# Kernel optimization log

Measured on AMD Instinct MI355X. Metric: run time of the kernel, lower is better.

Reference implementation:

```python
import jax, jax.numpy as jnp
import numpy as np

# Dimensions
B, T = 128, 512
H = 256            # lstm_hiddens; encoder width is 2*H
LIN = 200          # linear_hiddens (LSTMCell input size)
PD, WD = 50, 20    # pos_dims, wordlen_dims
PN, WN = 32, 8     # pos_num, wordlen_num (word len clipped to 7)
SP = 58            # segpos_num
APP_ID = 0         # id of the APP action (forbidden at t=0)


def setup_inputs() -> dict:
    key = jax.random.key(0)
    ks = jax.random.split(key, 13)
    enc = jax.random.normal(ks[0], (B, T, 2 * H), dtype=jnp.float32)
    sep_mask = jax.random.randint(ks[1], (B, T), 0, 2, dtype=jnp.int32)
    sep_mask = sep_mask.at[:, 0].set(1)  # first action is always SEP (APP forbidden at t=0)
    pos_ids = jax.random.randint(ks[2], (B, T), 0, PN, dtype=jnp.int32)
    length = jax.random.randint(ks[3], (B,), T // 2, T + 1, dtype=jnp.int32)
    s = 0.05
    pos_emb = jax.random.normal(ks[4], (PN, PD), dtype=jnp.float32) * s
    wordlen_emb = jax.random.normal(ks[5], (WN, WD), dtype=jnp.float32) * s
    fc_W = jax.random.normal(ks[6], (LIN, PD + 2 * H + WD), dtype=jnp.float32) * s
    fc_b = jax.random.normal(ks[7], (LIN,), dtype=jnp.float32) * s
    W_ih = jax.random.normal(ks[8], (4 * H, LIN), dtype=jnp.float32) * s
    W_hh = jax.random.normal(ks[9], (4 * H, H), dtype=jnp.float32) * s
    b_ih = jax.random.normal(ks[10], (4 * H,), dtype=jnp.float32) * s
    b_hh = jax.random.normal(ks[11], (4 * H,), dtype=jnp.float32) * s
    combine_W = jax.random.normal(ks[12], (SP, 3 * H), dtype=jnp.float32) * s
    return {"encoder_output": enc, "sep_mask": sep_mask, "pos_ids": pos_ids,
            "length": length, "pos_emb": pos_emb, "wordlen_emb": wordlen_emb,
            "fc_W": fc_W, "fc_b": fc_b, "W_ih": W_ih, "W_hh": W_hh,
            "b_ih": b_ih, "b_hh": b_hh, "combine_W": combine_W}


def reference(encoder_output, sep_mask, pos_ids, length, pos_emb, wordlen_emb,
              fc_W, fc_b, W_ih, W_hh, b_ih, b_hh, combine_W):
    b, t, h2 = encoder_output.shape
    h = h2 // 2
    idx = jnp.arange(t, dtype=jnp.int32)

    # last SEP position strictly before t (word start of the in-progress word)
    sep_pos = jnp.where(sep_mask > 0, idx[None, :], 0)            # [B,T]
    cmax = jax.lax.cummax(sep_pos, axis=1)                        # last sep <= t
    last_sep = jnp.concatenate(
        [jnp.zeros((b, 1), jnp.int32), cmax[:, :-1]], axis=1)     # last sep < t

    wlen = idx[None, :] - last_sep                                # [B,T]; >=1 for t>=1
    wlen_safe = jnp.maximum(wlen, 1)
    wlen_id = jnp.minimum(wlen_safe, 7)                           # clip: len>6 -> 7

    # mean of encoder states over the current word [last_sep, t) via cumsum
    csum = jnp.concatenate(
        [jnp.zeros((b, 1, h2), encoder_output.dtype),
         jnp.cumsum(encoder_output, axis=1)], axis=1)             # [B,T+1,2H]
    start_sum = jnp.take_along_axis(csum, last_sep[:, :, None], axis=1)
    word_avg = (csum[:, :t] - start_sum) / wlen_safe[:, :, None].astype(encoder_output.dtype)

    last_pos = jnp.take_along_axis(pos_ids, last_sep, axis=1)     # [B,T]
    feats = jnp.concatenate(
        [pos_emb[last_pos], word_avg, wordlen_emb[wlen_id]], axis=-1)  # [B,T,PD+2H+WD]
    z = jnp.tanh(jnp.einsum('btf,lf->btl', feats, fc_W) + fc_b)   # [B,T,LIN]
    z = z.at[:, 0].set(0.0)                                       # step 0 input is zeros

    # LSTMCell recurrence over time (torch gate order: i, f, g, o)
    def step(carry, zt):
        hh, cc = carry
        g = zt @ W_ih.T + b_ih + hh @ W_hh.T + b_hh               # [B,4H]
        i, f, gg, o = jnp.split(g, 4, axis=-1)
        cc = jax.nn.sigmoid(f) * cc + jax.nn.sigmoid(i) * jnp.tanh(gg)
        hh = jax.nn.sigmoid(o) * jnp.tanh(cc)
        return (hh, cc), hh

    h0 = jnp.zeros((b, h), encoder_output.dtype)
    _, hs = jax.lax.scan(step, (h0, h0), jnp.swapaxes(z, 0, 1))   # hs: [T,B,H]
    hs = jnp.swapaxes(hs, 0, 1)                                   # [B,T,H]

    v = jnp.concatenate([hs, encoder_output], axis=-1)            # [B,T,3H]
    logits = jnp.einsum('btv,sv->bts', v, combine_W)              # [B,T,SP]
    logits = logits.at[:, 0, APP_ID].set(-1e30)                   # forbid APP at t=0 (in-place, no grad)
    valid = (idx[None, :] < length[:, None])[:, :, None]
    logits = jnp.where(valid, logits, 0.0)                        # pad steps emit zeros
    return logits.reshape(b * t, SP)
```

## Files before the change

### kernel.cpp

```cpp
#include <hip/hip_runtime.h>

typedef unsigned short ushort_t;
typedef unsigned int uint32;
typedef __attribute__((ext_vector_type(8))) short short8;
typedef __attribute__((ext_vector_type(4))) short short4v;
typedef __attribute__((ext_vector_type(4))) float floatx4;
typedef __attribute__((ext_vector_type(2))) float float2v;
typedef __attribute__((ext_vector_type(8))) int intx8;

#define B_    128
#define T_    512
#define H_    256
#define H2_   512
#define LIN_  200
#define LINP_ 224
#define G4_   1024
#define SP_   58
#define BT_   (B_*T_)

#define OFF_LS     0UL
#define OFF_LP     262144UL
#define OFF_WID    524288UL
#define OFF_INV    786432UL
#define OFF_POSW   1212416UL
#define OFF_WLW    1238016UL
#define OFF_BIASG  1244416UL
#define OFF_WHH    1248512UL
#define OFF_WIH    1772800UL
#define OFF_WENC   2231552UL
#define OFF_COMBW  2436352UL
#define OFF_ECW    2525440UL
#define OFF_Z      28739840UL
#define OFF_GPERM  58099968UL
#define OFF_VBF    192317696UL

__device__ __forceinline__ ushort_t f2bf(float x){
  uint32 u = __float_as_uint(x);
  u += 0x7fffu + ((u >> 16) & 1u);
  return (ushort_t)(u >> 16);
}
__device__ __forceinline__ float bf2f(ushort_t v){
  return __uint_as_float(((uint32)v) << 16);
}
__device__ __forceinline__ float fsig(float x){
  return __builtin_amdgcn_rcpf(1.0f + __expf(-x));
}
__device__ __forceinline__ float ftanh(float x){
  return 1.0f - 2.0f * __builtin_amdgcn_rcpf(1.0f + __expf(2.0f * x));
}

__global__ __launch_bounds__(512) void k_scan(const int* __restrict__ sep, const int* __restrict__ pos_ids,
                       int* __restrict__ ls, int* __restrict__ lp,
                       int* __restrict__ wid, float* __restrict__ inv){
  int b = blockIdx.x, t = threadIdx.x;
  __shared__ int sm[512];
  int v = (sep[b*T_ + t] > 0) ? t : 0;
  sm[t] = v;
  __syncthreads();
  #pragma unroll
  for (int off = 1; off < 512; off <<= 1){
    int o = (t >= off) ? sm[t - off] : 0;
    __syncthreads();
    v = (o > v) ? o : v;
    sm[t] = v;
    __syncthreads();
  }
  int l = (t == 0) ? 0 : sm[t - 1];
  int wlen = t - l;
  int wsv  = (wlen < 1) ? 1 : wlen;
  ls[b*T_ + t]  = l;
  lp[b*T_ + t]  = pos_ids[b*T_ + l];
  wid[b*T_ + t] = (wsv > 7) ? 7 : wsv;
  inv[b*T_ + t] = 1.0f / (float)wsv;
}

__global__ __launch_bounds__(256) void k_encbf(const float* __restrict__ enc, ushort_t* __restrict__ vbf){
  const long total = (long)BT_ * 128;
  for (long i = (long)blockIdx.x * 256 + threadIdx.x; i < total; i += 2048L * 256){
    floatx4 v = ((const floatx4*)enc)[i];
    long row = i >> 7;
    int c4 = (int)(i & 127);
    int b = (int)(row >> 9), t = (int)(row & (T_-1));
    short4v pk;
    pk[0] = (short)f2bf(v[0]); pk[1] = (short)f2bf(v[1]);
    pk[2] = (short)f2bf(v[2]); pk[3] = (short)f2bf(v[3]);
    *(short4v*)(void*)(vbf + ((long)t * B_ + b) * 768 + 256 + c4*4) = pk;
  }
}

__global__ __launch_bounds__(256) void k_small(
    const float* __restrict__ pos_emb, const float* __restrict__ wl_emb,
    const float* __restrict__ fcW, const float* __restrict__ W_ih,
    const float* __restrict__ W_hh, const float* __restrict__ b_ih,
    const float* __restrict__ b_hh, const float* __restrict__ combW,
    float* __restrict__ posW, float* __restrict__ wlW, float* __restrict__ biasg,
    char* __restrict__ whh8, ushort_t* __restrict__ wih,
    ushort_t* __restrict__ wenc, ushort_t* __restrict__ combwb){
  int idx = blockIdx.x * 256 + threadIdx.x;
  if (idx < 6400){
    int p = idx / 200, l = idx % 200;
    float s = 0.f;
    for (int d = 0; d < 50; d++) s += pos_emb[p*50 + d] * fcW[l*582 + d];
    posW[idx] = s; return;
  }
  idx -= 6400;
  if (idx < 1600){
    int w = idx / 200, l = idx % 200;
    float s = 0.f;
    for (int d = 0; d < 20; d++) s += wl_emb[w*20 + d] * fcW[l*582 + 562 + d];
    wlW[idx] = s; return;
  }
  idx -= 1600;
  if (idx < 1024){ biasg[idx] = b_ih[idx] + b_hh[idx]; return; }
  idx -= 1024;
  if (idx < 262144){
    int p8 = __builtin_amdgcn_cvt_pk_fp8_f32(W_hh[idx], W_hh[idx], 0, false);
    whh8[idx] = (char)(p8 & 0xff);
    return;
  }
  idx -= 262144;
  if (idx < 229376){
    int n = idx / 224, k = idx % 224;
    wih[idx] = (k < 200) ? f2bf(W_ih[n*200 + k]) : (ushort_t)0;
    return;
  }
  idx -= 229376;
  if (idx < 102400){
    int l = idx / 512, c = idx % 512;
    wenc[idx] = f2bf(fcW[l*582 + 50 + c]); return;
  }
  idx -= 102400;
  if (idx < 44544){ combwb[idx] = f2bf(combW[idx]); return; }
}

template<int EPI>
__global__ __launch_bounds__(256) void k_gemm(
    const ushort_t* __restrict__ A, long lda,
    const ushort_t* __restrict__ Bm, int K, int Nvalid,
    void* __restrict__ Cout, const float* __restrict__ bias, const int* __restrict__ len){
  __shared__ __attribute__((aligned(16))) ushort_t As[64][48];
  __shared__ __attribute__((aligned(16))) ushort_t Bs[64][48];
  int tid  = threadIdx.x;
  int lane = tid & 63, wave = tid >> 6;
  int u = lane & 15, quad = lane >> 4;
  int mh = wave >> 1, nh = wave & 1;
  long m0 = (long)blockIdx.y * 64;
  int  n0 = blockIdx.x * 64;
  int lrow = tid >> 2;
  int lcol = (tid & 3) * 8;
  const ushort_t* Arow = A + (m0 + lrow) * lda + lcol;
  bool bvalid = (n0 + lrow) < Nvalid;
  const ushort_t* Brow = Bm + (long)(n0 + lrow) * K + lcol;
  floatx4 acc[2][2] = {};
  for (int k = 0; k < K; k += 32){
    short8 av = *(const short8*)(const void*)(Arow + k);
    short8 bv = {0,0,0,0,0,0,0,0};
    if (bvalid) bv = *(const short8*)(const void*)(Brow + k);
    __syncthreads();
    *(short8*)(void*)&As[lrow][lcol] = av;
    *(short8*)(void*)&Bs[lrow][lcol] = bv;
    __syncthreads();
    short8 a0 = *(const short8*)(const void*)&As[mh*32 + u][quad*8];
    short8 a1 = *(const short8*)(const void*)&As[mh*32 + 16 + u][quad*8];
    short8 b0 = *(const short8*)(const void*)&Bs[nh*32 + u][quad*8];
    short8 b1 = *(const short8*)(const void*)&Bs[nh*32 + 16 + u][quad*8];
    acc[0][0] = __builtin_amdgcn_mfma_f32_16x16x32_bf16(a0, b0, acc[0][0], 0, 0, 0);
    acc[0][1] = __builtin_amdgcn_mfma_f32_16x16x32_bf16(a0, b1, acc[0][1], 0, 0, 0);
    acc[1][0] = __builtin_amdgcn_mfma_f32_16x16x32_bf16(a1, b0, acc[1][0], 0, 0, 0);
    acc[1][1] = __builtin_amdgcn_mfma_f32_16x16x32_bf16(a1, b1, acc[1][1], 0, 0, 0);
  }
  for (int mi = 0; mi < 2; mi++){
    for (int ni = 0; ni < 2; ni++){
      for (int r = 0; r < 4; r++){
        long m = m0 + mh*32 + mi*16 + quad*4 + r;
        int  n = n0 + nh*32 + ni*16 + u;
        float v = acc[mi][ni][r];
        if (EPI == 0){
          if (n < Nvalid) ((ushort_t*)Cout)[m * Nvalid + n] = f2bf(v);
        } else {
          if (n < Nvalid){
            int t = (int)(m >> 7); int b = (int)(m & 127);
            float o = (t < len[b]) ? v : 0.0f;
            if (t == 0 && n == 0) o = -1e30f;
            ((float*)Cout)[((long)b * T_ + t) * SP_ + n] = o;
          }
        }
      }
    }
  }
}

template<int EPI>
__global__ __launch_bounds__(512, 2) void k_big(
    const ushort_t* __restrict__ A, long lda,
    const ushort_t* __restrict__ Bm, int K, int Nvalid,
    void* __restrict__ Cout, const float* __restrict__ bias){
  __shared__ __attribute__((aligned(16))) ushort_t As[2][128][32];
  __shared__ __attribute__((aligned(16))) ushort_t Bs[2][256][32];
  int tid  = threadIdx.x;
  int lane = tid & 63, w = tid >> 6;
  int u = lane & 15, quad = lane >> 4;
  int wm = w >> 2, wn = w & 3;
  long m0 = (long)blockIdx.y * 128;
  int  n0 = blockIdx.x * 256;
  int sr = lane >> 2;
  int gp = lane & 3;
  int gl = gp ^ ((sr >> 1) & 3);
  int arow = w*16 + sr;
  const ushort_t* asrc = A + (m0 + arow) * lda + gl*8;
  int brow = w*32 + sr;
  const ushort_t* bsrc0 = Bm + (long)(n0 + brow) * K + gl*8;
  const ushort_t* bsrc1 = Bm + (long)(n0 + brow + 16) * K + gl*8;
  floatx4 acc[4][4] = {};

#define STAGEK(buf, kk) do{ \
    __builtin_amdgcn_global_load_lds( \
        (const __attribute__((address_space(1))) void*)(asrc + (kk)), \
        (__attribute__((address_space(3))) void*)((char*)&As[buf][0][0] + w*1024), 16, 0, 0); \
    __builtin_amdgcn_global_load_lds( \
        (const __attribute__((address_space(1))) void*)(bsrc0 + (kk)), \
        (__attribute__((address_space(3))) void*)((char*)&Bs[buf][0][0] + w*2048), 16, 0, 0); \
    __builtin_amdgcn_global_load_lds( \
        (const __attribute__((address_space(1))) void*)(bsrc1 + (kk)), \
        (__attribute__((address_space(3))) void*)((char*)&Bs[buf][0][0] + w*2048 + 1024), 16, 0, 0); \
  }while(0)

  STAGEK(0, 0);
  asm volatile("s_waitcnt vmcnt(0)\n\ts_barrier" ::: "memory");
  int nk = K >> 5;
  int cur = 0;
  for (int ks = 0; ks < nk; ks++){
    if (ks + 1 < nk) STAGEK(cur ^ 1, (ks + 1) << 5);
    short8 af[4], bfv[4];
    #pragma unroll
    for (int mi = 0; mi < 4; mi++){
      int row = wm*64 + mi*16 + u;
      int off = (row*64 + quad*16) ^ (((row >> 1) & 3) << 4);
      af[mi] = *(const short8*)(const void*)((const char*)&As[cur][0][0] + off);
    }
    #pragma unroll
    for (int ni = 0; ni < 4; ni++){
      int row = wn*64 + ni*16 + u;
      int off = (row*64 + quad*16) ^ (((row >> 1) & 3) << 4);
      bfv[ni] = *(const short8*)(const void*)((const char*)&Bs[cur][0][0] + off);
    }
    #pragma unroll
    for (int mi = 0; mi < 4; mi++)
      #pragma unroll
      for (int ni = 0; ni < 4; ni++)
        acc[mi][ni] = __builtin_amdgcn_mfma_f32_16x16x32_bf16(af[mi], bfv[ni], acc[mi][ni], 0, 0, 0);
    asm volatile("s_waitcnt vmcnt(0)\n\ts_barrier" ::: "memory");
    cur ^= 1;
  }
#undef STAGEK

  if (EPI == 1){
    #pragma unroll
    for (int mi = 0; mi < 4; mi++){
      #pragma unroll
      for (int ni = 0; ni < 4; ni++){
        long mm = m0 + wm*64 + mi*16 + quad*4;
        int n = n0 + wn*64 + ni*16 + u;
        float bv = bias[n];
        int t = (int)(mm >> 7);
        int b = (int)(mm & 127);
        int blk = b >> 2;
        int g = n >> 8, j = n & 255, ut = j & 15, jt = j >> 4;
        long idx = ((((long)t*32 + blk)*16 + jt)*4 + g)*64 + ut*4;
        short4v pk;
        #pragma unroll
        for (int r = 0; r < 4; r++) pk[r] = (short)f2bf(acc[mi][ni][r] + bv);
        *(short4v*)(void*)((ushort_t*)Cout + idx) = pk;
      }
    }
  } else {
    for (int mi = 0; mi < 4; mi++){
      for (int ni = 0; ni < 4; ni++){
        int n = n0 + wn*64 + ni*16 + u;
        if (n < Nvalid){
          #pragma unroll
          for (int r = 0; r < 4; r++){
            long m = m0 + wm*64 + mi*16 + quad*4 + r;
            ((ushort_t*)Cout)[m * Nvalid + n] = f2bf(acc[mi][ni][r]);
          }
        }
      }
    }
  }
}

__global__ __launch_bounds__(256) void k_cum200(ushort_t* __restrict__ E){
  int b = blockIdx.x;
  int c = threadIdx.x;
  if (c >= LIN_) return;
  float acc = 0.f;
  ushort_t* p = E + (long)b * LIN_ + c;
  const long rs = (long)B_ * LIN_;
  for (int t0 = 0; t0 < T_; t0 += 16){
    float vv[16];
    #pragma unroll
    for (int i = 0; i < 16; i++) vv[i] = bf2f(p[i*rs]);
    #pragma unroll
    for (int i = 0; i < 16; i++){ p[i*rs] = f2bf(acc); acc += vv[i]; }
    p += 16*rs;
  }
}

__global__ __launch_bounds__(256) void k_z(
    const ushort_t* __restrict__ CW, const int* __restrict__ ls, const int* __restrict__ lp,
    const int* __restrict__ wid, const float* __restrict__ inv,
    const float* __restrict__ posW, const float* __restrict__ wlW,
    const float* __restrict__ fcb, ushort_t* __restrict__ zbf){
  int l = threadIdx.x;
  if (l >= LINP_) return;
  float fb = (l < LIN_) ? fcb[l] : 0.f;
  #pragma unroll
  for (int i = 0; i < 8; i++){
    int m = blockIdx.x * 8 + i;
    int t = m >> 7;
    int b = m & 127;
    int ar = b * T_ + t;
    ushort_t o = 0;
    if (t != 0 && l < LIN_){
      int lsv = ls[ar];
      float x = bf2f(CW[(long)m * LIN_ + l]) - bf2f(CW[((long)lsv * B_ + b) * LIN_ + l]);
      x = x * inv[ar] + posW[lp[ar]*LIN_ + l] + wlW[wid[ar]*LIN_ + l] + fb;
      o = f2bf(ftanh(x));
    }
    zbf[(long)m * LINP_ + l] = o;
  }
}

__global__ __launch_bounds__(1024, 4) void k_rec(
    const ushort_t* __restrict__ Gperm, const char* __restrict__ whh8,
    ushort_t* __restrict__ vbf){
  int blk  = blockIdx.x;
  int tid  = threadIdx.x;
  int lane = tid & 63, w = tid >> 6;
  int u = lane & 15, quad = lane >> 4;
  __shared__ __attribute__((aligned(16))) char h8[2][16][272];
  for (int i = tid; i < (int)(sizeof(h8)/4); i += 1024) ((int*)h8)[i] = 0;

  intx8 wfx[4][2];
  #pragma unroll
  for (int g = 0; g < 4; g++){
    int grow = g*256 + w*16 + u;
    #pragma unroll
    for (int kc = 0; kc < 2; kc++){
      intx8 v = *(const intx8*)(const void*)(whh8 + (long)grow*256 + kc*128 + quad*32);
      asm volatile("" : "+v"(v));
      wfx[g][kc] = v;
    }
  }
  float c_reg = 0.f;
  floatx4 acc[4] = {};

  const ushort_t* gp0 = Gperm + ((long)blk*16 + w)*256 + (long)u*4 + quad;
  ushort_t gb[4];
  #pragma unroll
  for (int g = 0; g < 4; g++) gb[g] = gp0[g*64];

  for (int t = 0; t < T_; t++){
    #pragma unroll
    for (int g = 0; g < 4; g++) acc[g][0] = bf2f(gb[g]);
    asm volatile("s_waitcnt lgkmcnt(0)\n\ts_barrier" ::: "memory");
    intx8 af0 = *(const intx8*)(const void*)&h8[t & 1][u][quad*32];
    intx8 af1 = *(const intx8*)(const void*)&h8[t & 1][u][128 + quad*32];
    if (t && w < 4){
      ushort_t* vrow = vbf + ((long)(t-1) * B_ + blk*4 + w) * 768;
      uint32 p = *(const uint32*)(const void*)&h8[t & 1][4*w][lane*4];
      float2v lo = __builtin_amdgcn_cvt_pk_f32_fp8(p, false);
      float2v hi = __builtin_amdgcn_cvt_pk_f32_fp8(p, true);
      short4v pk;
      pk[0] = (short)f2bf(lo[0]); pk[1] = (short)f2bf(lo[1]);
      pk[2] = (short)f2bf(hi[0]); pk[3] = (short)f2bf(hi[1]);
      *(short4v*)(void*)&vrow[lane*4] = pk;
    }
    if (t + 1 < T_){
      const ushort_t* gp = gp0 + (long)(t+1)*131072;
      #pragma unroll
      for (int g = 0; g < 4; g++) gb[g] = gp[g*64];
    }
    acc[0] = __builtin_amdgcn_mfma_scale_f32_16x16x128_f8f6f4(
        af0, wfx[0][0], acc[0], 0, 0, 0, 0x7F7F7F7F, 0, 0x7F7F7F7F);
    acc[0] = __builtin_amdgcn_mfma_scale_f32_16x16x128_f8f6f4(
        af1, wfx[0][1], acc[0], 0, 0, 0, 0x7F7F7F7F, 0, 0x7F7F7F7F);
    acc[1] = __builtin_amdgcn_mfma_scale_f32_16x16x128_f8f6f4(
        af0, wfx[1][0], acc[1], 0, 0, 0, 0x7F7F7F7F, 0, 0x7F7F7F7F);
    acc[1] = __builtin_amdgcn_mfma_scale_f32_16x16x128_f8f6f4(
        af1, wfx[1][1], acc[1], 0, 0, 0, 0x7F7F7F7F, 0, 0x7F7F7F7F);
    float iv = fsig (acc[0][0]);
    float fv = fsig (acc[1][0]);
    acc[2] = __builtin_amdgcn_mfma_scale_f32_16x16x128_f8f6f4(
        af0, wfx[2][0], acc[2], 0, 0, 0, 0x7F7F7F7F, 0, 0x7F7F7F7F);
    acc[2] = __builtin_amdgcn_mfma_scale_f32_16x16x128_f8f6f4(
        af1, wfx[2][1], acc[2], 0, 0, 0, 0x7F7F7F7F, 0, 0x7F7F7F7F);
    acc[3] = __builtin_amdgcn_mfma_scale_f32_16x16x128_f8f6f4(
        af0, wfx[3][0], acc[3], 0, 0, 0, 0x7F7F7F7F, 0, 0x7F7F7F7F);
    acc[3] = __builtin_amdgcn_mfma_scale_f32_16x16x128_f8f6f4(
        af1, wfx[3][1], acc[3], 0, 0, 0, 0x7F7F7F7F, 0, 0x7F7F7F7F);
    float gv = ftanh(acc[2][0]);
    float ov = fsig (acc[3][0]);
    float c  = fv * c_reg + iv * gv;
    c_reg = c;
    float h  = ov * ftanh(c);
    int p8 = __builtin_amdgcn_cvt_pk_fp8_f32(h, h, 0, false);
    h8[(t+1)&1][quad*4][w*16 + u] = (char)(p8 & 0xff);
  }
  __syncthreads();
  if (w < 4){
    ushort_t* vrow = vbf + ((long)(T_-1) * B_ + blk*4 + w) * 768;
    uint32 p = *(const uint32*)(const void*)&h8[0][4*w][lane*4];
    float2v lo = __builtin_amdgcn_cvt_pk_f32_fp8(p, false);
    float2v hi = __builtin_amdgcn_cvt_pk_f32_fp8(p, true);
    short4v pk;
    pk[0] = (short)f2bf(lo[0]); pk[1] = (short)f2bf(lo[1]);
    pk[2] = (short)f2bf(hi[0]); pk[3] = (short)f2bf(hi[1]);
    *(short4v*)(void*)&vrow[lane*4] = pk;
  }
}

extern "C" void kernel_launch(void* const* d_in, const int* in_sizes, int n_in,
                              void* d_out, int out_size, void* d_ws, size_t ws_size,
                              hipStream_t stream){
  (void)in_sizes; (void)n_in; (void)out_size; (void)ws_size;
  const float* enc     = (const float*)d_in[0];
  const int*   sep     = (const int*)  d_in[1];
  const int*   pos_ids = (const int*)  d_in[2];
  const int*   len     = (const int*)  d_in[3];
  const float* pos_emb = (const float*)d_in[4];
  const float* wl_emb  = (const float*)d_in[5];
  const float* fcW     = (const float*)d_in[6];
  const float* fcb     = (const float*)d_in[7];
  const float* W_ih    = (const float*)d_in[8];
  const float* W_hh    = (const float*)d_in[9];
  const float* b_ih    = (const float*)d_in[10];
  const float* b_hh    = (const float*)d_in[11];
  const float* combW   = (const float*)d_in[12];

  char* ws = (char*)d_ws;
  int*      ls    = (int*)     (ws + OFF_LS);
  int*      lp    = (int*)     (ws + OFF_LP);
  int*      wid   = (int*)     (ws + OFF_WID);
  float*    inv   = (float*)   (ws + OFF_INV);
  float*    posW  = (float*)   (ws + OFF_POSW);
  float*    wlW   = (float*)   (ws + OFF_WLW);
  float*    biasg = (float*)   (ws + OFF_BIASG);
  char*     whh8  = (char*)    (ws + OFF_WHH);
  ushort_t* wih   = (ushort_t*)(ws + OFF_WIH);
  ushort_t* wenc  = (ushort_t*)(ws + OFF_WENC);
  ushort_t* combwb= (ushort_t*)(ws + OFF_COMBW);
  ushort_t* ecw   = (ushort_t*)(ws + OFF_ECW);
  ushort_t* zbf   = (ushort_t*)(ws + OFF_Z);
  ushort_t* gperm = (ushort_t*)(ws + OFF_GPERM);
  ushort_t* vbf   = (ushort_t*)(ws + OFF_VBF);

  k_scan<<<B_, 512, 0, stream>>>(sep, pos_ids, ls, lp, wid, inv);
  k_encbf<<<2048, 256, 0, stream>>>(enc, vbf);
  k_small<<<2530, 256, 0, stream>>>(pos_emb, wl_emb, fcW, W_ih, W_hh, b_ih, b_hh, combW,
                                    posW, wlW, biasg, whh8, wih, wenc, combwb);
  k_big<0><<<dim3(1, BT_/128), 512, 0, stream>>>(vbf + 256, 768L, wenc, 512, LIN_, ecw, nullptr);
  k_cum200<<<B_, 256, 0, stream>>>(ecw);
  k_z<<<BT_/8, 256, 0, stream>>>(ecw, ls, lp, wid, inv, posW, wlW, fcb, zbf);
  k_big<1><<<dim3(4, BT_/128), 512, 0, stream>>>(zbf, (long)LINP_, wih, LINP_, G4_, gperm, biasg);
  k_rec<<<32, 1024, 0, stream>>>(gperm, whh8, vbf);
  k_gemm<1><<<dim3(1, BT_/64), 256, 0, stream>>>(vbf, 768L, combwb, 768, SP_, d_out, nullptr, len);
}
```

Before: 823.0 us.

## Split recurrence into two launches and replace logits GEMM with LDS-pipelined kernel

The LSTM recurrence kernel is split into two phase launches that hand off cell and hidden state through workspace buffers. The final logits GEMM is replaced by a new kernel with 256-row tiles, double-buffered direct global-to-LDS loads and swizzled LDS reads, which cuts the number of blocks and improves reuse of the small combine weight. Splitting the recurrence adds a launch and a save/restore of state, and does not by itself add parallelism. It may be groundwork for overlapping the logits of the first half with the second-half recurrence.

```diff
diff --git a/kernel.cpp b/kernel.cpp
--- a/kernel.cpp
+++ b/kernel.cpp
@@ -22,6 +22,8 @@
 #define OFF_LP     262144UL
 #define OFF_WID    524288UL
 #define OFF_INV    786432UL
+#define OFF_CSAVE  1048576UL
+#define OFF_HSAVE  1179648UL
 #define OFF_POSW   1212416UL
 #define OFF_WLW    1238016UL
 #define OFF_BIASG  1244416UL
@@ -131,63 +133,6 @@
   }
   idx -= 102400;
   if (idx < 44544){ combwb[idx] = f2bf(combW[idx]); return; }
-}
-
-template<int EPI>
-__global__ __launch_bounds__(256) void k_gemm(
-    const ushort_t* __restrict__ A, long lda,
-    const ushort_t* __restrict__ Bm, int K, int Nvalid,
-    void* __restrict__ Cout, const float* __restrict__ bias, const int* __restrict__ len){
-  __shared__ __attribute__((aligned(16))) ushort_t As[64][48];
-  __shared__ __attribute__((aligned(16))) ushort_t Bs[64][48];
-  int tid  = threadIdx.x;
-  int lane = tid & 63, wave = tid >> 6;
-  int u = lane & 15, quad = lane >> 4;
-  int mh = wave >> 1, nh = wave & 1;
-  long m0 = (long)blockIdx.y * 64;
-  int  n0 = blockIdx.x * 64;
-  int lrow = tid >> 2;
-  int lcol = (tid & 3) * 8;
-  const ushort_t* Arow = A + (m0 + lrow) * lda + lcol;
-  bool bvalid = (n0 + lrow) < Nvalid;
-  const ushort_t* Brow = Bm + (long)(n0 + lrow) * K + lcol;
-  floatx4 acc[2][2] = {};
-  for (int k = 0; k < K; k += 32){
-    short8 av = *(const short8*)(const void*)(Arow + k);
-    short8 bv = {0,0,0,0,0,0,0,0};
-    if (bvalid) bv = *(const short8*)(const void*)(Brow + k);
-    __syncthreads();
-    *(short8*)(void*)&As[lrow][lcol] = av;
-    *(short8*)(void*)&Bs[lrow][lcol] = bv;
-    __syncthreads();
-    short8 a0 = *(const short8*)(const void*)&As[mh*32 + u][quad*8];
-    short8 a1 = *(const short8*)(const void*)&As[mh*32 + 16 + u][quad*8];
-    short8 b0 = *(const short8*)(const void*)&Bs[nh*32 + u][quad*8];
-    short8 b1 = *(const short8*)(const void*)&Bs[nh*32 + 16 + u][quad*8];
-    acc[0][0] = __builtin_amdgcn_mfma_f32_16x16x32_bf16(a0, b0, acc[0][0], 0, 0, 0);
-    acc[0][1] = __builtin_amdgcn_mfma_f32_16x16x32_bf16(a0, b1, acc[0][1], 0, 0, 0);
-    acc[1][0] = __builtin_amdgcn_mfma_f32_16x16x32_bf16(a1, b0, acc[1][0], 0, 0, 0);
-    acc[1][1] = __builtin_amdgcn_mfma_f32_16x16x32_bf16(a1, b1, acc[1][1], 0, 0, 0);
-  }
-  for (int mi = 0; mi < 2; mi++){
-    for (int ni = 0; ni < 2; ni++){
-      for (int r = 0; r < 4; r++){
-        long m = m0 + mh*32 + mi*16 + quad*4 + r;
-        int  n = n0 + nh*32 + ni*16 + u;
-        float v = acc[mi][ni][r];
-        if (EPI == 0){
-          if (n < Nvalid) ((ushort_t*)Cout)[m * Nvalid + n] = f2bf(v);
-        } else {
-          if (n < Nvalid){
-            int t = (int)(m >> 7); int b = (int)(m & 127);
-            float o = (t < len[b]) ? v : 0.0f;
-            if (t == 0 && n == 0) o = -1e30f;
-            ((float*)Cout)[((long)b * T_ + t) * SP_ + n] = o;
-          }
-        }
-      }
-    }
-  }
 }
 
 template<int EPI>
@@ -289,6 +234,84 @@
   }
 }
 
+__global__ __launch_bounds__(512, 2) void k_logit(
+    const ushort_t* __restrict__ A,
+    const ushort_t* __restrict__ Bm,
+    float* __restrict__ Cout, const int* __restrict__ len){
+  __shared__ __attribute__((aligned(16))) ushort_t As[2][256][32];
+  __shared__ __attribute__((aligned(16))) ushort_t Bs[2][64][32];
+  int tid  = threadIdx.x;
+  int lane = tid & 63, w = tid >> 6;
+  int u = lane & 15, quad = lane >> 4;
+  int wm = w >> 1, wn = w & 1;
+  long m0 = (long)blockIdx.x * 256;
+  int sr = lane >> 2;
+  int gp = lane & 3;
+  int gl = gp ^ ((sr >> 1) & 3);
+  const ushort_t* asrc0 = A + (m0 + w*32 + sr) * 768 + gl*8;
+  const ushort_t* asrc1 = A + (m0 + w*32 + 16 + sr) * 768 + gl*8;
+  const ushort_t* bsrc  = Bm + (long)(w*16 + sr) * 768 + gl*8;
+  floatx4 acc[4][2] = {};
+
+#define STG(buf, kk) do{ \
+    __builtin_amdgcn_global_load_lds( \
+        (const __attribute__((address_space(1))) void*)(asrc0 + (kk)), \
+        (__attribute__((address_space(3))) void*)((char*)&As[buf][0][0] + w*2048), 16, 0, 0); \
+    __builtin_amdgcn_global_load_lds( \
+        (const __attribute__((address_space(1))) void*)(asrc1 + (kk)), \
+        (__attribute__((address_space(3))) void*)((char*)&As[buf][0][0] + w*2048 + 1024), 16, 0, 0); \
+    if (w < 4) __builtin_amdgcn_global_load_lds( \
+        (const __attribute__((address_space(1))) void*)(bsrc + (kk)), \
+        (__attribute__((address_space(3))) void*)((char*)&Bs[buf][0][0] + w*1024), 16, 0, 0); \
+  }while(0)
+
+  STG(0, 0);
+  asm volatile("s_waitcnt vmcnt(0)\n\ts_barrier" ::: "memory");
+  int cur = 0;
+  for (int ks = 0; ks < 24; ks++){
+    if (ks + 1 < 24) STG(cur ^ 1, (ks + 1) << 5);
+    short8 af[4], bfv[2];
+    #pragma unroll
+    for (int mi = 0; mi < 4; mi++){
+      int row = wm*64 + mi*16 + u;
+      int off = (row*64 + quad*16) ^ (((row >> 1) & 3) << 4);
+      af[mi] = *(const short8*)(const void*)((const char*)&As[cur][0][0] + off);
+    }
+    #pragma unroll
+    for (int ni = 0; ni < 2; ni++){
+      int row = wn*32 + ni*16 + u;
+      int off = (row*64 + quad*16) ^ (((row >> 1) & 3) << 4);
+      bfv[ni] = *(const short8*)(const void*)((const char*)&Bs[cur][0][0] + off);
+    }
+    #pragma unroll
+    for (int mi = 0; mi < 4; mi++)
+      #pragma unroll
+      for (int ni = 0; ni < 2; ni++)
+        acc[mi][ni] = __builtin_amdgcn_mfma_f32_16x16x32_bf16(af[mi], bfv[ni], acc[mi][ni], 0, 0, 0);
+    asm volatile("s_waitcnt vmcnt(0)\n\ts_barrier" ::: "memory");
+    cur ^= 1;
+  }
+#undef STG
+
+  #pragma unroll
+  for (int mi = 0; mi < 4; mi++){
+    #pragma unroll
+    for (int ni = 0; ni < 2; ni++){
+      int n = wn*32 + ni*16 + u;
+      if (n < SP_){
+        #pragma unroll
+        for (int r = 0; r < 4; r++){
+          long m = m0 + wm*64 + mi*16 + quad*4 + r;
+          int t = (int)(m >> 7); int b = (int)(m & 127);
+          float o = (t < len[b]) ? acc[mi][ni][r] : 0.0f;
+          if (t == 0 && n == 0) o = -1e30f;
+          Cout[((long)b * T_ + t) * SP_ + n] = o;
+        }
+      }
+    }
+  }
+}
+
 __global__ __launch_bounds__(256) void k_cum200(ushort_t* __restrict__ E){
   int b = blockIdx.x;
   int c = threadIdx.x;
@@ -331,9 +354,10 @@
   }
 }
 
-__global__ __launch_bounds__(1024, 4) void k_rec(
+template<int PHASE>
+__global__ __launch_bounds__(1024, 4) void k_rec2(
     const ushort_t* __restrict__ Gperm, const char* __restrict__ whh8,
-    ushort_t* __restrict__ vbf){
+    ushort_t* __restrict__ vbf, float* __restrict__ csave, char* __restrict__ hsave){
   int blk  = blockIdx.x;
   int tid  = threadIdx.x;
   int lane = tid & 63, w = tid >> 6;
@@ -352,15 +376,27 @@
       wfx[g][kc] = v;
     }
   }
-  float c_reg = 0.f;
+  float c_reg;
   floatx4 acc[4] = {};
+  const int T0 = PHASE ? (T_/2) : 0;
+  const int T1 = PHASE ? T_ : (T_/2);
+  if (PHASE == 0){
+    c_reg = 0.f;
+    __syncthreads();
+  } else {
+    c_reg = csave[((blk*16 + w) << 6) + lane];
+    __syncthreads();
+    if (w < 4)
+      ((uint32*)&h8[0][4*w][0])[lane] = ((const uint32*)(hsave + (blk*4 + w)*256))[lane];
+    __syncthreads();
+  }
 
   const ushort_t* gp0 = Gperm + ((long)blk*16 + w)*256 + (long)u*4 + quad;
   ushort_t gb[4];
   #pragma unroll
-  for (int g = 0; g < 4; g++) gb[g] = gp0[g*64];
-
-  for (int t = 0; t < T_; t++){
+  for (int g = 0; g < 4; g++) gb[g] = gp0[(long)T0*131072 + g*64];
+
+  for (int t = T0; t < T1; t++){
     #pragma unroll
     for (int g = 0; g < 4; g++) acc[g][0] = bf2f(gb[g]);
     asm volatile("s_waitcnt lgkmcnt(0)\n\ts_barrier" ::: "memory");
@@ -408,15 +444,21 @@
     h8[(t+1)&1][quad*4][w*16 + u] = (char)(p8 & 0xff);
   }
   __syncthreads();
-  if (w < 4){
-    ushort_t* vrow = vbf + ((long)(T_-1) * B_ + blk*4 + w) * 768;
-    uint32 p = *(const uint32*)(const void*)&h8[0][4*w][lane*4];
-    float2v lo = __builtin_amdgcn_cvt_pk_f32_fp8(p, false);
-    float2v hi = __builtin_amdgcn_cvt_pk_f32_fp8(p, true);
-    short4v pk;
-    pk[0] = (short)f2bf(lo[0]); pk[1] = (short)f2bf(lo[1]);
-    pk[2] = (short)f2bf(hi[0]); pk[3] = (short)f2bf(hi[1]);
-    *(short4v*)(void*)&vrow[lane*4] = pk;
+  if (PHASE == 0){
+    if (w < 4)
+      ((uint32*)(hsave + (blk*4 + w)*256))[lane] = *(const uint32*)&h8[0][4*w][lane*4];
+    csave[((blk*16 + w) << 6) + lane] = c_reg;
+  } else {
+    if (w < 4){
+      ushort_t* vrow = vbf + ((long)(T_-1) * B_ + blk*4 + w) * 768;
+      uint32 p = *(const uint32*)(const void*)&h8[0][4*w][lane*4];
+      float2v lo = __builtin_amdgcn_cvt_pk_f32_fp8(p, false);
+      float2v hi = __builtin_amdgcn_cvt_pk_f32_fp8(p, true);
+      short4v pk;
+      pk[0] = (short)f2bf(lo[0]); pk[1] = (short)f2bf(lo[1]);
+      pk[2] = (short)f2bf(hi[0]); pk[3] = (short)f2bf(hi[1]);
+      *(short4v*)(void*)&vrow[lane*4] = pk;
+    }
   }
 }
 
@@ -443,6 +485,8 @@
   int*      lp    = (int*)     (ws + OFF_LP);
   int*      wid   = (int*)     (ws + OFF_WID);
   float*    inv   = (float*)   (ws + OFF_INV);
+  float*    csave = (float*)   (ws + OFF_CSAVE);
+  char*     hsave = (char*)    (ws + OFF_HSAVE);
   float*    posW  = (float*)   (ws + OFF_POSW);
   float*    wlW   = (float*)   (ws + OFF_WLW);
   float*    biasg = (float*)   (ws + OFF_BIASG);
@@ -463,6 +507,7 @@
   k_cum200<<<B_, 256, 0, stream>>>(ecw);
   k_z<<<BT_/8, 256, 0, stream>>>(ecw, ls, lp, wid, inv, posW, wlW, fcb, zbf);
   k_big<1><<<dim3(4, BT_/128), 512, 0, stream>>>(zbf, (long)LINP_, wih, LINP_, G4_, gperm, biasg);
-  k_rec<<<32, 1024, 0, stream>>>(gperm, whh8, vbf);
-  k_gemm<1><<<dim3(1, BT_/64), 256, 0, stream>>>(vbf, 768L, combwb, 768, SP_, d_out, nullptr, len);
-}
+  k_rec2<0><<<32, 1024, 0, stream>>>(gperm, whh8, vbf, csave, hsave);
+  k_rec2<1><<<32, 1024, 0, stream>>>(gperm, whh8, vbf, csave, hsave);
+  k_logit<<<BT_/256, 512, 0, stream>>>(vbf, combwb, (float*)d_out, len);
+}
```

Result: slower. 849.8 us (+3.3%).
